# Optimization experiments

Measured on AMD Instinct MI355X. Metric: run time of the kernel, lower is better.

The kernel has to match this reference:

```python
import jax, jax.numpy as jnp
import numpy as np

GATE_SLOPE = 10.0
ALPHA = 0.8
KH = KW = 3
PAD = 1
STRIDE = 1


def setup_inputs() -> dict:
    key = jax.random.key(0)
    ks = jax.random.split(key, 7)
    B, Cin, H, W = 4, 16, 32, 32
    Cout, NB = 32, 3
    pshape = (Cout, Cin, NB, KH, KW)
    x = jax.random.normal(ks[0], (B, Cin, H, W), dtype=jnp.float32)
    k = jax.random.uniform(ks[1], pshape, dtype=jnp.float32) * 2.0 + 0.5
    Ec = jax.random.uniform(ks[2], pshape, dtype=jnp.float32) * 2.0 + 0.5
    Ps = jax.random.uniform(ks[3], pshape, dtype=jnp.float32) * 1.5 + 0.5
    bias = jax.random.normal(ks[4], pshape, dtype=jnp.float32) * 0.1
    coef = jax.random.normal(ks[5], pshape, dtype=jnp.float32)
    out_bias = jnp.zeros((Cout,), dtype=jnp.float32)
    return {"x": x, "k": k, "Ec": Ec, "Ps": Ps, "bias": bias, "coef": coef, "out_bias": out_bias}


def _unfold(x):
    # x: (B, Cin, H, W) -> (B, Cin, kH, kW, L) like F.unfold with pad/stride
    B, Cin, H, W = x.shape
    Hout = (H + 2 * PAD - KH) // STRIDE + 1
    Wout = (W + 2 * PAD - KW) // STRIDE + 1
    xp = jnp.pad(x, ((0, 0), (0, 0), (PAD, PAD), (PAD, PAD)))
    patches = jnp.stack(
        [xp[:, :, i:i + Hout * STRIDE:STRIDE, j:j + Wout * STRIDE:STRIDE]
         for i in range(KH) for j in range(KW)], axis=2)  # (B,Cin,kH*kW,Hout,Wout)
    return patches.reshape(B, Cin, KH, KW, Hout * Wout), Hout, Wout


def reference(x, k, Ec, Ps, bias, coef, out_bias):
    B, Cin, H, W = x.shape
    Cout = k.shape[0]
    x_exp, Hout, Wout = _unfold(x)  # (B,Cin,kH,kW,L)
    # stateful=False: prev_x = stop_gradient(x), branch = 1.0
    dx = x_exp - jax.lax.stop_gradient(x_exp)
    is_up = jax.nn.sigmoid(GATE_SLOPE * dx)  # value 0.5, nonzero grad path
    # broadcast axes: x -> (B,1,Cin,1,kH,kW,L); params -> (1,Cout,Cin,NB,kH,kW,1)
    x7 = x_exp[:, None, :, None]
    up7 = is_up[:, None, :, None]
    kc, Ecc, Psc, bc, cc = (p[None, ..., None] for p in (k, Ec, Ps, bias, coef))
    crossed_pos = jax.nn.sigmoid(GATE_SLOPE * (x7 - Ecc))
    crossed_neg = jax.nn.sigmoid(GATE_SLOPE * (-x7 - Ecc))
    sw_up = up7 * crossed_pos
    sw_lo = (1.0 - up7) * crossed_neg
    branch = 1.0
    target_sign = sw_up - sw_lo + (1.0 - sw_up - sw_lo) * branch
    branch_momentum = ALPHA * branch + (1.0 - ALPHA) * target_sign
    shifted = x7 + Ecc * branch_momentum
    basis = Psc * jnp.tanh(kc * shifted) + bc
    out = jnp.sum(basis * cc, axis=(2, 3, 4, 5))  # (B,Cout,L)
    out = out.reshape(B, Cout, Hout, Wout) + out_bias[None, :, None, None]
    return out
```

## Files before the change

### kernel.cpp

```cpp
#include <hip/hip_runtime.h>

#define LOG2E 1.4426950408889634f
#define C1 (10.0f * LOG2E)

__global__ __launch_bounds__(256, 4) void fused_kernel(
    const float* __restrict__ x, const float* __restrict__ kk,
    const float* __restrict__ Ec, const float* __restrict__ Ps,
    const float* __restrict__ bias, const float* __restrict__ coef,
    const float* __restrict__ out_bias, float* __restrict__ out) {
    __shared__ float2 sX[2176];
    __shared__ float4 sP[432];
    __shared__ float  sW[432];
    __shared__ float  red[256];
    __shared__ float  wK0[4];

    const int bid = blockIdx.x, tid = threadIdx.x;
    const int chunk = bid & 15;
    const int co    = (bid >> 4) & 31;
    const int b     = bid >> 9;

    for (int t = tid; t < 2176; t += 256) {
        int ci  = t / 136;
        int rem = t - ci * 136;
        int r   = rem / 34;
        int c   = rem - r * 34;
        int row = chunk * 2 + r - 1;
        int col = c - 1;
        float xv = 0.f;
        if ((unsigned)row < 32u && (unsigned)col < 32u)
            xv = x[((b * 16 + ci) << 10) + (row << 5) + col];
        sX[t] = make_float2(xv, __builtin_amdgcn_exp2f(C1 * xv));
    }

    float kpart = 0.f;
    for (int t = tid; t < 432; t += 256) {
        int ci = t / 27;
        int r2 = t - ci * 27;
        int j  = r2 / 3;
        int nb = r2 - j * 3;
        int i  = co * 432 + ci * 27 + nb * 9 + j;
        float e  = Ec[i];
        float zk = 2.0f * LOG2E * kk[i];
        float a  = zk * e;
        float ps = Ps[i], cf = coef[i];
        sP[t] = make_float4(__builtin_amdgcn_exp2f(C1 * e), zk, a, 0.2f * a);
        sW[t] = 2.0f * ps * cf;
        kpart += cf * (ps + bias[i]);
    }
    #pragma unroll
    for (int off = 32; off >= 1; off >>= 1) kpart += __shfl_down(kpart, off, 64);
    if ((tid & 63) == 0) wK0[tid >> 6] = kpart;
    __syncthreads();

    const int px = tid & 63;
    const int w  = px & 31;
    const int hr = px >> 5;
    const int cb = (tid >> 6) << 2;

    float a0 = 0.f, a1 = 0.f, a2 = 0.f;
    #pragma unroll
    for (int i = 0; i < 4; ++i) {
        const float2* xw = &sX[(cb + i) * 136 + hr * 34 + w];
        float2 X[9];
        #pragma unroll
        for (int j = 0; j < 9; ++j)
            X[j] = xw[(j / 3) * 34 + (j % 3)];
        const float4* pc = &sP[(cb + i) * 27];
        const float*  wc = &sW[(cb + i) * 27];
        #pragma unroll
        for (int j = 0; j < 9; ++j) {
            const float xv = X[j].x, E1 = X[j].y;
            const float4 P0 = pc[j * 3 + 0];
            const float4 P1 = pc[j * 3 + 1];
            const float4 P2 = pc[j * 3 + 2];
            const float w0 = wc[j * 3 + 0];
            const float w1 = wc[j * 3 + 1];
            const float w2v = wc[j * 3 + 2];
            float d0 = fminf(__builtin_fmaf(E1, P0.x, 1.f), 0x1p40f);
            float d1 = fminf(__builtin_fmaf(E1, P1.x, 1.f), 0x1p40f);
            float d2 = fminf(__builtin_fmaf(E1, P2.x, 1.f), 0x1p40f);
            float q01 = d0 * d1, q12 = d1 * d2, q02 = d0 * d2;
            float rp = __builtin_amdgcn_rcpf(q01 * d2);
            float t0 = __builtin_fmaf(P0.y, xv, P0.z);
            float t1 = __builtin_fmaf(P1.y, xv, P1.z);
            float t2 = __builtin_fmaf(P2.y, xv, P2.z);
            float m0 = P0.w * q12, m1 = P1.w * q02, m2 = P2.w * q01;
            float u0 = __builtin_fmaf(-m0, rp, t0);
            float u1 = __builtin_fmaf(-m1, rp, t1);
            float u2 = __builtin_fmaf(-m2, rp, t2);
            float e0 = __builtin_amdgcn_exp2f(u0);
            float e1 = __builtin_amdgcn_exp2f(u1);
            float e2 = __builtin_amdgcn_exp2f(u2);
            float f0 = fminf(1.f + e0, 0x1p42f);
            float f1 = fminf(1.f + e1, 0x1p42f);
            float f2 = fminf(1.f + e2, 0x1p42f);
            float s01 = f0 * f1, s12 = f1 * f2, s02 = f0 * f2;
            float rq = __builtin_amdgcn_rcpf(s01 * f2);
            float n0 = w0 * s12, n1 = w1 * s02, n2 = w2v * s01;
            a0 = __builtin_fmaf(-n0, rq, a0);
            a1 = __builtin_fmaf(-n1, rq, a1);
            a2 = __builtin_fmaf(-n2, rq, a2);
        }
    }
    red[tid] = a0 + a1 + a2;
    __syncthreads();
    if (tid < 64) {
        float r = red[tid] + red[tid + 64] + red[tid + 128] + red[tid + 192];
        float k0 = wK0[0] + wK0[1] + wK0[2] + wK0[3] + out_bias[co];
        int o = ((b * 32 + co) << 10) + (chunk << 6) + tid;
        out[o] = r + k0;
    }
}

extern "C" void kernel_launch(void* const* d_in, const int* in_sizes, int n_in,
                              void* d_out, int out_size, void* d_ws, size_t ws_size,
                              hipStream_t stream) {
    const float* x        = (const float*)d_in[0];
    const float* k        = (const float*)d_in[1];
    const float* Ec       = (const float*)d_in[2];
    const float* Ps       = (const float*)d_in[3];
    const float* bias     = (const float*)d_in[4];
    const float* coef     = (const float*)d_in[5];
    const float* out_bias = (const float*)d_in[6];
    float* out = (float*)d_out;

    fused_kernel<<<2048, 256, 0, stream>>>(x, k, Ec, Ps, bias, coef, out_bias, out);
}
```

Measured before the change: 30.40 us.

## Process four output rows per block and simplify the gate reciprocal math

Each block now covers four rows instead of two. The grid halves to 1024 blocks, and each thread computes two pixels, reusing the same parameter loads from shared memory. The three products of d0·d1·d2 plus one shared reciprocal are replaced by three direct reciprocals, removing multiplies and the clamp. The reduction buffer reuses the sX shared memory. This lowers LDS traffic and per-block setup per pixel, at the cost of higher register pressure and fewer blocks for occupancy.

```diff
diff --git a/kernel.cpp b/kernel.cpp
--- a/kernel.cpp
+++ b/kernel.cpp
@@ -8,23 +8,22 @@
     const float* __restrict__ Ec, const float* __restrict__ Ps,
     const float* __restrict__ bias, const float* __restrict__ coef,
     const float* __restrict__ out_bias, float* __restrict__ out) {
-    __shared__ float2 sX[2176];
+    __shared__ float2 sX[3264];
     __shared__ float4 sP[432];
     __shared__ float  sW[432];
-    __shared__ float  red[256];
     __shared__ float  wK0[4];
 
     const int bid = blockIdx.x, tid = threadIdx.x;
-    const int chunk = bid & 15;
-    const int co    = (bid >> 4) & 31;
-    const int b     = bid >> 9;
+    const int chunk = bid & 7;
+    const int co    = (bid >> 3) & 31;
+    const int b     = bid >> 8;
 
-    for (int t = tid; t < 2176; t += 256) {
-        int ci  = t / 136;
-        int rem = t - ci * 136;
+    for (int t = tid; t < 3264; t += 256) {
+        int ci  = t / 204;
+        int rem = t - ci * 204;
         int r   = rem / 34;
         int c   = rem - r * 34;
-        int row = chunk * 2 + r - 1;
+        int row = chunk * 4 + r - 1;
         int col = c - 1;
         float xv = 0.f;
         if ((unsigned)row < 32u && (unsigned)col < 32u)
@@ -57,58 +56,77 @@
     const int hr = px >> 5;
     const int cb = (tid >> 6) << 2;
 
-    float a0 = 0.f, a1 = 0.f, a2 = 0.f;
+    float a00 = 0.f, a01 = 0.f, a02 = 0.f;
+    float a10 = 0.f, a11 = 0.f, a12 = 0.f;
     #pragma unroll
     for (int i = 0; i < 4; ++i) {
-        const float2* xw = &sX[(cb + i) * 136 + hr * 34 + w];
-        float2 X[9];
-        #pragma unroll
-        for (int j = 0; j < 9; ++j)
-            X[j] = xw[(j / 3) * 34 + (j % 3)];
-        const float4* pc = &sP[(cb + i) * 27];
-        const float*  wc = &sW[(cb + i) * 27];
+        const int ci = cb + i;
+        const float2* xw = &sX[ci * 204 + hr * 34 + w];
+        float2 X0[9], X1[9];
         #pragma unroll
         for (int j = 0; j < 9; ++j) {
-            const float xv = X[j].x, E1 = X[j].y;
+            X0[j] = xw[(j / 3) * 34 + (j % 3)];
+            X1[j] = xw[(j / 3) * 34 + (j % 3) + 68];
+        }
+        const float4* pc = &sP[ci * 27];
+        const float*  wc = &sW[ci * 27];
+        #pragma unroll
+        for (int j = 0; j < 9; ++j) {
             const float4 P0 = pc[j * 3 + 0];
             const float4 P1 = pc[j * 3 + 1];
             const float4 P2 = pc[j * 3 + 2];
             const float w0 = wc[j * 3 + 0];
             const float w1 = wc[j * 3 + 1];
             const float w2v = wc[j * 3 + 2];
-            float d0 = fminf(__builtin_fmaf(E1, P0.x, 1.f), 0x1p40f);
-            float d1 = fminf(__builtin_fmaf(E1, P1.x, 1.f), 0x1p40f);
-            float d2 = fminf(__builtin_fmaf(E1, P2.x, 1.f), 0x1p40f);
-            float q01 = d0 * d1, q12 = d1 * d2, q02 = d0 * d2;
-            float rp = __builtin_amdgcn_rcpf(q01 * d2);
-            float t0 = __builtin_fmaf(P0.y, xv, P0.z);
-            float t1 = __builtin_fmaf(P1.y, xv, P1.z);
-            float t2 = __builtin_fmaf(P2.y, xv, P2.z);
-            float m0 = P0.w * q12, m1 = P1.w * q02, m2 = P2.w * q01;
-            float u0 = __builtin_fmaf(-m0, rp, t0);
-            float u1 = __builtin_fmaf(-m1, rp, t1);
-            float u2 = __builtin_fmaf(-m2, rp, t2);
-            float e0 = __builtin_amdgcn_exp2f(u0);
-            float e1 = __builtin_amdgcn_exp2f(u1);
-            float e2 = __builtin_amdgcn_exp2f(u2);
-            float f0 = fminf(1.f + e0, 0x1p42f);
-            float f1 = fminf(1.f + e1, 0x1p42f);
-            float f2 = fminf(1.f + e2, 0x1p42f);
-            float s01 = f0 * f1, s12 = f1 * f2, s02 = f0 * f2;
-            float rq = __builtin_amdgcn_rcpf(s01 * f2);
-            float n0 = w0 * s12, n1 = w1 * s02, n2 = w2v * s01;
-            a0 = __builtin_fmaf(-n0, rq, a0);
-            a1 = __builtin_fmaf(-n1, rq, a1);
-            a2 = __builtin_fmaf(-n2, rq, a2);
+            {
+                const float xv = X0[j].x, E1 = X0[j].y;
+                float cn0 = __builtin_amdgcn_rcpf(__builtin_fmaf(E1, P0.x, 1.f));
+                float cn1 = __builtin_amdgcn_rcpf(__builtin_fmaf(E1, P1.x, 1.f));
+                float cn2 = __builtin_amdgcn_rcpf(__builtin_fmaf(E1, P2.x, 1.f));
+                float u0 = __builtin_fmaf(-P0.w, cn0, __builtin_fmaf(P0.y, xv, P0.z));
+                float u1 = __builtin_fmaf(-P1.w, cn1, __builtin_fmaf(P1.y, xv, P1.z));
+                float u2 = __builtin_fmaf(-P2.w, cn2, __builtin_fmaf(P2.y, xv, P2.z));
+                float f0 = fminf(1.f + __builtin_amdgcn_exp2f(u0), 0x1p42f);
+                float f1 = fminf(1.f + __builtin_amdgcn_exp2f(u1), 0x1p42f);
+                float f2 = fminf(1.f + __builtin_amdgcn_exp2f(u2), 0x1p42f);
+                float s01 = f0 * f1, s12 = f1 * f2, s02 = f0 * f2;
+                float rq = __builtin_amdgcn_rcpf(s01 * f2);
+                a00 = __builtin_fmaf(-(w0 * s12), rq, a00);
+                a01 = __builtin_fmaf(-(w1 * s02), rq, a01);
+                a02 = __builtin_fmaf(-(w2v * s01), rq, a02);
+            }
+            {
+                const float xv = X1[j].x, E1 = X1[j].y;
+                float cn0 = __builtin_amdgcn_rcpf(__builtin_fmaf(E1, P0.x, 1.f));
+                float cn1 = __builtin_amdgcn_rcpf(__builtin_fmaf(E1, P1.x, 1.f));
+                float cn2 = __builtin_amdgcn_rcpf(__builtin_fmaf(E1, P2.x, 1.f));
+                float u0 = __builtin_fmaf(-P0.w, cn0, __builtin_fmaf(P0.y, xv, P0.z));
+                float u1 = __builtin_fmaf(-P1.w, cn1, __builtin_fmaf(P1.y, xv, P1.z));
+                float u2 = __builtin_fmaf(-P2.w, cn2, __builtin_fmaf(P2.y, xv, P2.z));
+                float f0 = fminf(1.f + __builtin_amdgcn_exp2f(u0), 0x1p42f);
+                float f1 = fminf(1.f + __builtin_amdgcn_exp2f(u1), 0x1p42f);
+                float f2 = fminf(1.f + __builtin_amdgcn_exp2f(u2), 0x1p42f);
+                float s01 = f0 * f1, s12 = f1 * f2, s02 = f0 * f2;
+                float rq = __builtin_amdgcn_rcpf(s01 * f2);
+                a10 = __builtin_fmaf(-(w0 * s12), rq, a10);
+                a11 = __builtin_fmaf(-(w1 * s02), rq, a11);
+                a12 = __builtin_fmaf(-(w2v * s01), rq, a12);
+            }
         }
     }
-    red[tid] = a0 + a1 + a2;
+
+    __syncthreads();
+    float* sR = (float*)sX;
+    sR[tid]       = a00 + a01 + a02;
+    sR[tid + 256] = a10 + a11 + a12;
     __syncthreads();
     if (tid < 64) {
-        float r = red[tid] + red[tid + 64] + red[tid + 128] + red[tid + 192];
+        float r0 = sR[tid] + sR[tid + 64] + sR[tid + 128] + sR[tid + 192];
+        float r1 = sR[tid + 256] + sR[tid + 320] + sR[tid + 384] + sR[tid + 448];
         float k0 = wK0[0] + wK0[1] + wK0[2] + wK0[3] + out_bias[co];
-        int o = ((b * 32 + co) << 10) + (chunk << 6) + tid;
-        out[o] = r + k0;
+        int o0 = ((b * 32 + co) << 10) + ((chunk * 4 + (tid >> 5)) << 5) + (tid & 31);
+        out[o0]      = r0 + k0;
+        out[o0 + 64] = r1 + k0;
     }
 }
 
@@ -124,5 +142,5 @@
     const float* out_bias = (const float*)d_in[6];
     float* out = (float*)d_out;
 
-    fused_kernel<<<2048, 256, 0, stream>>>(x, k, Ec, Ps, bias, coef, out_bias, out);
+    fused_kernel<<<1024, 256, 0, stream>>>(x, k, Ec, Ps, bias, coef, out_bias, out);
 }
```

Result: faster. 29.71 us (-2.3%).
